# Kernel tuning notes

Hardware: AMD Instinct MI355X
Metric: run time of the kernel (lower is better)

Reference implementation:

```python
import jax, jax.numpy as jnp
import numpy as np

B, N_PER, F = 8, 4096, 64
RATIO, RADIUS, K = 0.25, 0.2, 64
S = int(N_PER * RATIO)  # 1024 samples per cloud
NEG = -1e30


def setup_inputs() -> dict:
    key = jax.random.key(0)
    ks = jax.random.split(key, 8)
    pos = jax.random.uniform(ks[0], (B * N_PER, 3), dtype=jnp.float32)
    x = jax.random.normal(ks[1], (B * N_PER, F), dtype=jnp.float32)
    batch = jnp.repeat(jnp.arange(B, dtype=jnp.int32), N_PER)
    W1 = jax.random.normal(ks[2], (F + 3, 128), dtype=jnp.float32) * 0.05
    b1 = jnp.zeros((128,), jnp.float32)
    W2 = jax.random.normal(ks[3], (128, 128), dtype=jnp.float32) * 0.05
    b2 = jnp.zeros((128,), jnp.float32)
    W3 = jax.random.normal(ks[4], (128, 256), dtype=jnp.float32) * 0.05
    b3 = jnp.zeros((256,), jnp.float32)
    return {"x": x, "pos": pos, "batch": batch,
            "W1": W1, "b1": b1, "W2": W2, "b2": b2, "W3": W3, "b3": b3}


def _fps_single(p):
    """Farthest point sampling on one cloud p:[N,3] -> S int32 indices (seed idx 0)."""
    d0 = jnp.sum((p - p[0]) ** 2, axis=-1)  # [N]

    def step(min_d, _):
        nxt = jnp.argmax(min_d).astype(jnp.int32)
        d = jnp.sum((p - p[nxt]) ** 2, axis=-1)
        return jnp.minimum(min_d, d), nxt

    _, rest = jax.lax.scan(step, d0, None, length=S - 1)
    return jnp.concatenate([jnp.zeros((1,), jnp.int32), rest])


def reference(x, pos, batch, W1, b1, W2, b2, W3, b3):
    pos_b = pos.reshape(B, N_PER, 3)
    x_b = x.reshape(B, N_PER, F)
    batch_b = batch.reshape(B, N_PER)

    # --- FPS sampling (sequential scan, vmapped over clouds) ---
    idx = jax.vmap(_fps_single)(pos_b)                                  # [B,S]
    pos_s = jnp.take_along_axis(pos_b, idx[..., None], axis=1)          # [B,S,3]

    # --- radius neighbor search: nearest K within RADIUS (deterministic) ---
    d2 = jnp.sum((pos_s[:, :, None, :] - pos_b[:, None, :, :]) ** 2, -1)  # [B,S,N]
    neg = jnp.where(d2 <= RADIUS ** 2, -d2, NEG)
    vals, nbr = jax.lax.top_k(neg, K)                                   # [B,S,K]
    valid = vals > NEG / 2                                              # [B,S,K]

    # --- gather neighbor features / positions ---
    x_j = jnp.take_along_axis(x_b[:, None], nbr[..., None], axis=2)     # [B,S,K,F]
    pos_j = jnp.take_along_axis(pos_b[:, None], nbr[..., None], axis=2) # [B,S,K,3]
    rel = pos_j - pos_s[:, :, None, :]                                  # [B,S,K,3]

    # --- edge MLP (Lin+ReLU per PyG PointNetConv local_nn) ---
    h = jnp.concatenate([x_j, rel], axis=-1)                            # [B,S,K,F+3]
    h = jax.nn.relu(h @ W1 + b1)
    h = jax.nn.relu(h @ W2 + b2)
    h = jax.nn.relu(h @ W3 + b3)                                        # [B,S,K,256]

    # --- scatter-max aggregation over neighbors ---
    h = jnp.where(valid[..., None], h, NEG)
    out = jnp.max(h, axis=2)                                            # [B,S,256]
    out = jnp.where(out > NEG / 2, out, 0.0)

    x1 = out.reshape(B * S, -1)
    pos1 = pos_s.reshape(B * S, 3)
    batch1 = jnp.take_along_axis(batch_b, idx, axis=1).reshape(-1)
    return x1, pos1, batch1
```

## Files before the change

kernel.cpp:

```cpp
#include <hip/hip_runtime.h>
#include <hip/hip_bf16.h>
#include <stdint.h>

#define NPER 4096
#define NCLOUD 8
#define FD 64
#define SS 1024
#define NBK 64
#define CAP 512

typedef unsigned int u32;
typedef unsigned long long u64;
typedef __attribute__((ext_vector_type(8))) short short8v;
typedef __attribute__((ext_vector_type(8))) unsigned short ushort8v;
typedef __attribute__((ext_vector_type(4))) float f32x4;

__device__ __forceinline__ float fadd(float a, float b){ return __fadd_rn(a,b); }
__device__ __forceinline__ float fsub(float a, float b){ return __fsub_rn(a,b); }
__device__ __forceinline__ float fmul(float a, float b){ return __fmul_rn(a,b); }
__device__ __forceinline__ float dist2(float ax,float ay,float az,float bx,float by,float bz){
  float dx=fsub(ax,bx), dy=fsub(ay,by), dz=fsub(az,bz);
  return fadd(fadd(fmul(dx,dx),fmul(dy,dy)),fmul(dz,dz));
}
__device__ __forceinline__ unsigned short f2b(float v){
  __hip_bfloat16 h = __float2bfloat16(v);
  return *reinterpret_cast<unsigned short*>(&h);
}

template<int CTRL, int RMASK>
__device__ __forceinline__ float dppmaxf(float v){
  int t = __builtin_amdgcn_update_dpp(0, __float_as_int(v), CTRL, RMASK, 0xf, false);
  return fmaxf(v, __int_as_float(t));
}

#define LOADG(q, j0, j1, j2, j3) { \
    const float4* pv = (const float4*)(pb + (size_t)(base + q*4)*3); \
    float4 v0=pv[0], v1=pv[1], v2=pv[2]; \
    x##j0=v0.x; y##j0=v0.y; z##j0=v0.z; \
    x##j1=v0.w; y##j1=v1.x; z##j1=v1.y; \
    x##j2=v1.z; y##j2=v1.w; z##j2=v2.x; \
    x##j3=v2.y; y##j3=v2.z; z##j3=v2.w; \
    float4 c0; c0.x=x##j0; c0.y=y##j0; c0.z=z##j0; c0.w=0.f; spt[base+q*4+0]=c0; \
    float4 c1; c1.x=x##j1; c1.y=y##j1; c1.z=z##j1; c1.w=0.f; spt[base+q*4+1]=c1; \
    float4 c2; c2.x=x##j2; c2.y=y##j2; c2.z=z##j2; c2.w=0.f; spt[base+q*4+2]=c2; \
    float4 c3; c3.x=x##j3; c3.y=y##j3; c3.z=z##j3; c3.w=0.f; spt[base+q*4+3]=c3; \
  }
#define DINIT(j) m##j = dist2(x##j,y##j,z##j,p0x,p0y,p0z);
#define DUPD(j)  { float d = dist2(x##j,y##j,z##j,pnx,pny,pnz); m##j = fminf(m##j,d); }
#define ARGMAX16() { \
      bool c; float w0,w1,w2,w3,w4,w5,w6,w7; int i0,i1,i2,i3,i4,i5,i6,i7; \
      c=m1>m0;   w0=c?m1:m0;   i0=base+(c?1:0); \
      c=m3>m2;   w1=c?m3:m2;   i1=base+(c?3:2); \
      c=m5>m4;   w2=c?m5:m4;   i2=base+(c?5:4); \
      c=m7>m6;   w3=c?m7:m6;   i3=base+(c?7:6); \
      c=m9>m8;   w4=c?m9:m8;   i4=base+(c?9:8); \
      c=m11>m10; w5=c?m11:m10; i5=base+(c?11:10); \
      c=m13>m12; w6=c?m13:m12; i6=base+(c?13:12); \
      c=m15>m14; w7=c?m15:m14; i7=base+(c?15:14); \
      c=w1>w0; w0=c?w1:w0; i0=c?i1:i0; \
      c=w3>w2; w2=c?w3:w2; i2=c?i3:i2; \
      c=w5>w4; w4=c?w5:w4; i4=c?i5:i4; \
      c=w7>w6; w6=c?w7:w6; i6=c?i7:i6; \
      c=w2>w0; w0=c?w2:w0; i0=c?i2:i0; \
      c=w6>w4; w4=c?w6:w4; i4=c?i6:i4; \
      c=w4>w0; bv=c?w4:w0; bidx=c?i4:i0; \
    }
#define FPS_ITER(IT, WX, WY, WZ) { \
    float rv = bv; \
    rv = dppmaxf<0x121,0xf>(rv); \
    rv = dppmaxf<0x122,0xf>(rv); \
    rv = dppmaxf<0x124,0xf>(rv); \
    rv = dppmaxf<0x128,0xf>(rv); \
    rv = dppmaxf<0x142,0xa>(rv); \
    rv = dppmaxf<0x143,0xc>(rv); \
    const float wv = __int_as_float(__builtin_amdgcn_readlane(__float_as_int(rv), 63)); \
    u64 em = __ballot(bv == wv); \
    const int wl = __ffsll(em) - 1; \
    const int par = (IT) & 1; \
    const u32 se = (u32)((IT) >> 1); \
    if (lane == wl) \
      skey[par][w] = ((u64)__float_as_uint(wv)<<32) | ((u64)se<<12) | (u64)(u32)(4095 - bidx); \
    u64 k0,k1,k2,k3; \
    for (;;) { \
      k0 = skey[par][0]; k1 = skey[par][1]; k2 = skey[par][2]; k3 = skey[par][3]; \
      u32 c0 = (((u32)k0)>>12)^se, c1 = (((u32)k1)>>12)^se; \
      u32 c2 = (((u32)k2)>>12)^se, c3 = (((u32)k3)>>12)^se; \
      if ((c0|c1|c2|c3) == 0u) break; \
    } \
    u64 ka = k0>k1?k0:k1, kb2 = k2>k3?k2:k3; \
    u64 km = ka>kb2?ka:kb2; \
    const int nxt = 4095 - (int)(km & 0xFFFull); \
    const float4 c = spt[nxt]; \
    const float pnx = __int_as_float(__builtin_amdgcn_readfirstlane(__float_as_int(c.x))); \
    const float pny = __int_as_float(__builtin_amdgcn_readfirstlane(__float_as_int(c.y))); \
    const float pnz = __int_as_float(__builtin_amdgcn_readfirstlane(__float_as_int(c.z))); \
    const bool mine = (t == ((IT) & 255)); \
    WX = mine ? pnx : WX; \
    WY = mine ? pny : WY; \
    WZ = mine ? pnz : WZ; \
    DUPD(0) DUPD(1) DUPD(2) DUPD(3) DUPD(4) DUPD(5) DUPD(6) DUPD(7) \
    DUPD(8) DUPD(9) DUPD(10) DUPD(11) DUPD(12) DUPD(13) DUPD(14) DUPD(15) \
    ARGMAX16() \
  }

__global__ __launch_bounds__(256, 1) void k_fps(const float* __restrict__ pos,
    float* __restrict__ pos_s, float* __restrict__ out_pos1, float* __restrict__ out_b1){
  __shared__ __align__(16) float4 spt[NPER];
  __shared__ volatile __align__(16) u64 skey[2][4];
  const int b = blockIdx.x;
  const int t = threadIdx.x;
  const int w = t >> 6, lane = t & 63;
  const float* pb = pos + (size_t)b*NPER*3;
  const int base = t*16;
  float x0,x1,x2,x3,x4,x5,x6,x7,x8,x9,x10,x11,x12,x13,x14,x15;
  float y0,y1,y2,y3,y4,y5,y6,y7,y8,y9,y10,y11,y12,y13,y14,y15;
  float z0,z1,z2,z3,z4,z5,z6,z7,z8,z9,z10,z11,z12,z13,z14,z15;
  float m0,m1,m2,m3,m4,m5,m6,m7,m8,m9,m10,m11,m12,m13,m14,m15;
  LOADG(0, 0, 1, 2, 3)
  LOADG(1, 4, 5, 6, 7)
  LOADG(2, 8, 9, 10, 11)
  LOADG(3, 12, 13, 14, 15)
  const float p0x=pb[0], p0y=pb[1], p0z=pb[2];
  DINIT(0) DINIT(1) DINIT(2) DINIT(3) DINIT(4) DINIT(5) DINIT(6) DINIT(7)
  DINIT(8) DINIT(9) DINIT(10) DINIT(11) DINIT(12) DINIT(13) DINIT(14) DINIT(15)
  float bv; int bidx;
  ARGMAX16()
  if (t < 8) skey[t>>2][t&3] = 0xFFFFF000ull;
  float wx0=p0x, wy0=p0y, wz0=p0z;
  float wx1=0.f, wy1=0.f, wz1=0.f;
  float wx2=0.f, wy2=0.f, wz2=0.f;
  float wx3=0.f, wy3=0.f, wz3=0.f;
  for (int i=t;i<SS;i+=256) out_b1[b*SS+i] = (float)b;
  __syncthreads();
  for (int it=1;   it<256;  ++it) FPS_ITER(it, wx0, wy0, wz0)
  for (int it=256; it<512;  ++it) FPS_ITER(it, wx1, wy1, wz1)
  for (int it=512; it<768;  ++it) FPS_ITER(it, wx2, wy2, wz2)
  for (int it=768; it<1024; ++it) FPS_ITER(it, wx3, wy3, wz3)
  {
    const size_t g = (size_t)b*SS;
    size_t o = (g + t)*3;
    pos_s[o]=wx0; pos_s[o+1]=wy0; pos_s[o+2]=wz0;
    out_pos1[o]=wx0; out_pos1[o+1]=wy0; out_pos1[o+2]=wz0;
    o = (g + 256 + t)*3;
    pos_s[o]=wx1; pos_s[o+1]=wy1; pos_s[o+2]=wz1;
    out_pos1[o]=wx1; out_pos1[o+1]=wy1; out_pos1[o+2]=wz1;
    o = (g + 512 + t)*3;
    pos_s[o]=wx2; pos_s[o+1]=wy2; pos_s[o+2]=wz2;
    out_pos1[o]=wx2; out_pos1[o+1]=wy2; out_pos1[o+2]=wz2;
    o = (g + 768 + t)*3;
    pos_s[o]=wx3; pos_s[o+1]=wy3; pos_s[o+2]=wz3;
    out_pos1[o]=wx3; out_pos1[o+1]=wy3; out_pos1[o+2]=wz3;
  }
}

__global__ __launch_bounds__(256) void k_nbr(const float* __restrict__ pos,
    const float* __restrict__ pos_s, unsigned short* __restrict__ nbr){
  __shared__ float sxx[NPER], syy[NPER], szz[NPER];
  __shared__ u64 lst[4][CAP];
  __shared__ int cnt[4];
  const int t = threadIdx.x;
  const int w = t>>6, lane = t&63;
  const int gid0 = blockIdx.x*4;
  const int b = gid0 >> 10;
  const float* pb = pos + (size_t)b*NPER*3;
  for (int i=t;i<NPER;i+=256){
    sxx[i]=pb[i*3+0]; syy[i]=pb[i*3+1]; szz[i]=pb[i*3+2];
  }
  if (t<4) cnt[t]=0;
  __syncthreads();
  const int gid = gid0 + w;
  const float qx=pos_s[(size_t)gid*3+0], qy=pos_s[(size_t)gid*3+1], qz=pos_s[(size_t)gid*3+2];
  for (int i0=0;i0<NPER;i0+=64){
    int p = i0 + lane;
    float d = dist2(qx,qy,qz,sxx[p],syy[p],szz[p]);
    bool in = (d <= 0.04f);
    u64 m = __ballot(in);
    if (m){
      int tot = __popcll(m);
      int bse = 0;
      if (lane==0) bse = atomicAdd(&cnt[w], tot);
      bse = __shfl(bse, 0, 64);
      if (in){
        int o = bse + __popcll(m & ((1ull<<lane)-1ull));
        if (o < CAP) lst[w][o] = ((u64)__float_as_uint(d)<<12) | (u64)(u32)p;
      }
    }
  }
  int n = cnt[w];
  if (n > CAP) n = CAP;
  unsigned short outv = 0xFFFFu;
  if (n <= 64){
    if (lane < n) outv = (unsigned short)(lst[w][lane] & 0xFFFull);
  } else {
    for (int r=0;r<64;++r){
      u64 bk = ~0ull; int bp = -1;
      for (int i=lane;i<n;i+=64){
        u64 v = lst[w][i];
        bool lt = v < bk;
        bk = lt ? v : bk;
        bp = lt ? i : bp;
      }
      u64 rk = bk;
      #pragma unroll
      for (int off=32; off>=1; off>>=1){
        u64 o = __shfl_xor(rk, off, 64);
        rk = (o < rk) ? o : rk;
      }
      if (bk == rk) lst[w][bp] = ~0ull;
      if (lane == r) outv = (unsigned short)(rk & 0xFFFull);
    }
  }
  nbr[(size_t)gid*NBK + lane] = outv;
}

__global__ __launch_bounds__(256) void k_wconv(const float* __restrict__ W1,
    const float* __restrict__ W2, const float* __restrict__ W3,
    unsigned short* __restrict__ Wt1, unsigned short* __restrict__ Wt2,
    unsigned short* __restrict__ Wt3){
  int t = blockIdx.x*256 + threadIdx.x;
  if (t < 16384){
    int n = t>>7, k = t&127;
    Wt1[t] = f2b(k < 67 ? W1[k*128+n] : 0.f);
  } else if (t < 32768){
    int q = t - 16384; int n = q>>7, k = q&127;
    Wt2[q] = f2b(W2[k*128+n]);
  } else if (t < 65536){
    int q = t - 32768; int n = q>>7, k = q&127;
    Wt3[q] = f2b(W3[k*256+n]);
  }
}

__device__ __forceinline__ void load_w(const unsigned short* __restrict__ src,
    unsigned short* __restrict__ wb, int t){
  const int n = t>>1, hf = t&1;
  const char* srow = (const char*)(src + n*128 + hf*64);
  char* drow = (char*)wb + n*256;
  const u32 sw = (u32)(n&7)<<4;
  #pragma unroll
  for (int c=0;c<8;c++){
    ushort8v v = *(const ushort8v*)(srow + c*16);
    u32 colbyte = (u32)hf*128 + (u32)c*16;
    *(ushort8v*)(drow + (colbyte ^ sw)) = v;
  }
}

__device__ __forceinline__ void zero_acc(f32x4 acc[4][4]){
  #pragma unroll
  for (int i=0;i<4;i++){
    #pragma unroll
    for (int j=0;j<4;j++){
      f32x4 z = {0.f,0.f,0.f,0.f};
      acc[i][j] = z;
    }
  }
}

__device__ __forceinline__ void gemm_wave(const unsigned short* __restrict__ wb,
    const unsigned short* __restrict__ hb, int nh, int lane, int ksteps, f32x4 acc[4][4]){
  const int li = lane & 15;
  const int lg = lane >> 4;
  for (int kk=0; kk<ksteps; ++kk){
    const u32 colb = (u32)(kk*64 + lg*16);
    short8v af[4], bfv[4];
    #pragma unroll
    for (int mt=0;mt<4;mt++){
      int wr = nh*64 + mt*16 + li;
      af[mt] = *(const short8v*)((const char*)wb + wr*256 + (colb ^ ((u32)(wr&7)<<4)));
    }
    #pragma unroll
    for (int nt=0;nt<4;nt++){
      int er = nt*16 + li;
      bfv[nt] = *(const short8v*)((const char*)hb + er*256 + (colb ^ ((u32)(er&7)<<4)));
    }
    #pragma unroll
    for (int mt=0;mt<4;mt++){
      #pragma unroll
      for (int nt=0;nt<4;nt++){
        acc[mt][nt] = __builtin_amdgcn_mfma_f32_16x16x32_bf16(af[mt], bfv[nt], acc[mt][nt], 0, 0, 0);
      }
    }
  }
}

__device__ __forceinline__ void epi_store(f32x4 acc[4][4], const float* __restrict__ bias,
    unsigned short* __restrict__ hb, int nh, int lane){
  const int li = lane & 15;
  const int lg = lane >> 4;
  #pragma unroll
  for (int mt=0;mt<4;mt++){
    const int c0 = nh*64 + mt*16 + lg*4;
    const float4 bb = *(const float4*)(bias + c0);
    #pragma unroll
    for (int nt=0;nt<4;nt++){
      const int r = nt*16 + li;
      f32x4 a = acc[mt][nt];
      float v0 = fmaxf(a.x + bb.x, 0.f);
      float v1 = fmaxf(a.y + bb.y, 0.f);
      float v2 = fmaxf(a.z + bb.z, 0.f);
      float v3 = fmaxf(a.w + bb.w, 0.f);
      u64 pk = (u64)f2b(v0) | ((u64)f2b(v1)<<16) | ((u64)f2b(v2)<<32) | ((u64)f2b(v3)<<48);
      u32 colbyte = (u32)(c0*2);
      *(u64*)((char*)hb + r*256 + (colbyte ^ ((u32)(r&7)<<4))) = pk;
    }
  }
}

__device__ __forceinline__ void epi_out(f32x4 acc[4][4], const float* __restrict__ b3g,
    float* __restrict__ outx, u64 vmask, int pass, int nh, int lane, int gs){
  const int li = lane & 15;
  const int lg = lane >> 4;
  #pragma unroll
  for (int mt=0;mt<4;mt++){
    const int c0 = pass*128 + nh*64 + mt*16 + lg*4;
    const float4 bb = *(const float4*)(b3g + c0);
    float vals[4];
    #pragma unroll
    for (int i=0;i<4;i++){
      float v = -1e30f;
      #pragma unroll
      for (int nt=0;nt<4;nt++){
        const int r = nt*16 + li;
        const bool ok = (vmask >> r) & 1ull;
        const float a = acc[mt][nt][i];
        v = fmaxf(v, ok ? a : -1e30f);
      }
      #pragma unroll
      for (int off=1; off<16; off<<=1){
        v = fmaxf(v, __shfl_xor(v, off, 64));
      }
      float biasv = (i==0)?bb.x:((i==1)?bb.y:((i==2)?bb.z:bb.w));
      vals[i] = fmaxf(v + biasv, 0.f);
    }
    if (li==0){
      float4 o; o.x=vals[0]; o.y=vals[1]; o.z=vals[2]; o.w=vals[3];
      *(float4*)(outx + (size_t)gs*256 + c0) = o;
    }
  }
}

__global__ __launch_bounds__(256) void k_mlp(const float* __restrict__ xg,
    const float* __restrict__ pg, const float* __restrict__ pos_s,
    const unsigned short* __restrict__ nbrg,
    const unsigned short* __restrict__ Wt1, const unsigned short* __restrict__ Wt2,
    const unsigned short* __restrict__ Wt3,
    const float* __restrict__ b1g, const float* __restrict__ b2g,
    const float* __restrict__ b3g, float* __restrict__ outx){
  __shared__ __align__(16) unsigned short hbuf[2][64][128];
  __shared__ __align__(16) unsigned short wbuf[128*128];
  __shared__ float spos[2][4];
  __shared__ unsigned short snbr[2][64];
  __shared__ u64 svalid[2];
  const int t = threadIdx.x;
  const int s0 = blockIdx.x*2;
  const int b = s0 >> 10;
  {
    u64* p = (u64*)hbuf;
    #pragma unroll
    for (int i=0;i<16;i++) p[t + i*256] = 0ull;
  }
  if (t < 2){
    spos[t][0]=pos_s[(size_t)(s0+t)*3+0];
    spos[t][1]=pos_s[(size_t)(s0+t)*3+1];
    spos[t][2]=pos_s[(size_t)(s0+t)*3+2];
  }
  if (t < 128){
    const int s=t>>6, r=t&63;
    unsigned short nb = nbrg[(size_t)(s0+s)*NBK + r];
    snbr[s][r]=nb;
    u64 m = __ballot(nb != 0xFFFFu);
    if (r==0) svalid[s]=m;
  }
  __syncthreads();
  {
    const int s = t>>7, r=(t>>1)&63, hf=t&1;
    const unsigned short nb = snbr[s][r];
    char* drow = (char*)hbuf + (s*64+r)*256;
    const u32 sw = (u32)(r&7)<<4;
    if (nb != 0xFFFFu){
      const float4* xr = (const float4*)(xg + ((size_t)b*NPER + nb)*FD + hf*32);
      #pragma unroll
      for (int c=0;c<4;c++){
        float4 v0 = xr[2*c];
        float4 v1 = xr[2*c+1];
        ushort8v u;
        u[0]=f2b(v0.x); u[1]=f2b(v0.y); u[2]=f2b(v0.z); u[3]=f2b(v0.w);
        u[4]=f2b(v1.x); u[5]=f2b(v1.y); u[6]=f2b(v1.z); u[7]=f2b(v1.w);
        u32 colbyte = (u32)hf*64 + (u32)c*16;
        *(ushort8v*)(drow + (colbyte ^ sw)) = u;
      }
      if (hf){
        const size_t po = ((size_t)b*NPER + nb)*3;
        float rx = fsub(pg[po+0], spos[s][0]);
        float ry = fsub(pg[po+1], spos[s][1]);
        float rz = fsub(pg[po+2], spos[s][2]);
        u64 pk = (u64)f2b(rx) | ((u64)f2b(ry)<<16) | ((u64)f2b(rz)<<32);
        *(u64*)(drow + (128u ^ sw)) = pk;
      }
    }
  }
  load_w(Wt1, wbuf, t);
  __syncthreads();
  const int w = t>>6, lane = t&63;
  const int s = w>>1, nh = w&1;
  unsigned short* hb = &hbuf[s][0][0];
  f32x4 acc[4][4];
  zero_acc(acc);
  gemm_wave(wbuf, hb, nh, lane, 3, acc);
  __syncthreads();
  epi_store(acc, b1g, hb, nh, lane);
  load_w(Wt2, wbuf, t);
  __syncthreads();
  zero_acc(acc);
  gemm_wave(wbuf, hb, nh, lane, 4, acc);
  __syncthreads();
  epi_store(acc, b2g, hb, nh, lane);
  load_w(Wt3, wbuf, t);
  __syncthreads();
  zero_acc(acc);
  gemm_wave(wbuf, hb, nh, lane, 4, acc);
  const u64 vm = svalid[s];
  epi_out(acc, b3g, outx, vm, 0, nh, lane, s0+s);
  __syncthreads();
  load_w(Wt3 + 128*128, wbuf, t);
  __syncthreads();
  zero_acc(acc);
  gemm_wave(wbuf, hb, nh, lane, 4, acc);
  epi_out(acc, b3g, outx, vm, 1, nh, lane, s0+s);
}

extern "C" void kernel_launch(void* const* d_in, const int* in_sizes, int n_in,
                              void* d_out, int out_size, void* d_ws, size_t ws_size,
                              hipStream_t stream) {
  (void)in_sizes; (void)n_in; (void)out_size; (void)ws_size;
  const float* xg = (const float*)d_in[0];
  const float* pg = (const float*)d_in[1];
  const float* W1 = (const float*)d_in[3];
  const float* b1 = (const float*)d_in[4];
  const float* W2 = (const float*)d_in[5];
  const float* b2 = (const float*)d_in[6];
  const float* W3 = (const float*)d_in[7];
  const float* b3 = (const float*)d_in[8];
  float* outx = (float*)d_out;
  float* outp = outx + (size_t)8192*256;
  float* outb = outp + (size_t)8192*3;
  char* ws = (char*)d_ws;
  float* pos_s = (float*)ws;
  unsigned short* nbr = (unsigned short*)(ws + 98304);
  unsigned short* Wt1 = (unsigned short*)(ws + 98304 + 1048576);
  unsigned short* Wt2 = Wt1 + 16384;
  unsigned short* Wt3 = Wt2 + 16384;
  hipLaunchKernelGGL(k_fps, dim3(NCLOUD), dim3(256), 0, stream, pg, pos_s, outp, outb);
  hipLaunchKernelGGL(k_wconv, dim3(256), dim3(256), 0, stream, W1, W2, W3, Wt1, Wt2, Wt3);
  hipLaunchKernelGGL(k_nbr, dim3(8192/4), dim3(256), 0, stream, pg, pos_s, nbr);
  hipLaunchKernelGGL(k_mlp, dim3(8192/2), dim3(256), 0, stream,
                     xg, pg, pos_s, nbr, Wt1, Wt2, Wt3, b1, b2, b3, outx);
}
```

Measured before the change: 1.086 ms.

## Use barrier-based FPS reduction, fuse weight conversion, register top-k for neighbors

Replaces the volatile spin-wait on sequence-tagged shared keys in the FPS loop with a __syncthreads barrier per iteration. The weight bf16 conversion kernel is merged into the FPS launch as extra blocks to remove a launch. The neighbor selection gains a register-resident path for up to 256 candidates using a DPP-based 64-bit wave min, avoiding repeated LDS scans. The barrier per FPS step may cost more or less than spinning.

```diff
diff --git a/kernel.cpp b/kernel.cpp
--- a/kernel.cpp
+++ b/kernel.cpp
@@ -31,6 +31,14 @@
 __device__ __forceinline__ float dppmaxf(float v){
   int t = __builtin_amdgcn_update_dpp(0, __float_as_int(v), CTRL, RMASK, 0xf, false);
   return fmaxf(v, __int_as_float(t));
+}
+template<int CTRL, int RMASK>
+__device__ __forceinline__ void kmin_stage(u32& hi, u32& lo){
+  u32 hio = (u32)__builtin_amdgcn_update_dpp(-1, (int)hi, CTRL, RMASK, 0xf, false);
+  u32 loo = (u32)__builtin_amdgcn_update_dpp(-1, (int)lo, CTRL, RMASK, 0xf, false);
+  u64 ko = ((u64)hio<<32)|loo, k = ((u64)hi<<32)|lo;
+  bool g = ko < k;
+  hi = g?hio:hi; lo = g?loo:lo;
 }
 
 #define LOADG(q, j0, j1, j2, j3) { \
@@ -77,16 +85,11 @@
     u64 em = __ballot(bv == wv); \
     const int wl = __ffsll(em) - 1; \
     const int par = (IT) & 1; \
-    const u32 se = (u32)((IT) >> 1); \
     if (lane == wl) \
-      skey[par][w] = ((u64)__float_as_uint(wv)<<32) | ((u64)se<<12) | (u64)(u32)(4095 - bidx); \
-    u64 k0,k1,k2,k3; \
-    for (;;) { \
-      k0 = skey[par][0]; k1 = skey[par][1]; k2 = skey[par][2]; k3 = skey[par][3]; \
-      u32 c0 = (((u32)k0)>>12)^se, c1 = (((u32)k1)>>12)^se; \
-      u32 c2 = (((u32)k2)>>12)^se, c3 = (((u32)k3)>>12)^se; \
-      if ((c0|c1|c2|c3) == 0u) break; \
-    } \
+      skey[par][w] = ((u64)__float_as_uint(wv)<<32) | (u64)(u32)(4095 - bidx); \
+    __syncthreads(); \
+    const u64* kp = &skey[par][0]; \
+    u64 k0=kp[0], k1=kp[1], k2=kp[2], k3=kp[3]; \
     u64 ka = k0>k1?k0:k1, kb2 = k2>k3?k2:k3; \
     u64 km = ka>kb2?ka:kb2; \
     const int nxt = 4095 - (int)(km & 0xFFFull); \
@@ -104,9 +107,26 @@
   }
 
 __global__ __launch_bounds__(256, 1) void k_fps(const float* __restrict__ pos,
-    float* __restrict__ pos_s, float* __restrict__ out_pos1, float* __restrict__ out_b1){
+    float* __restrict__ pos_s, float* __restrict__ out_pos1, float* __restrict__ out_b1,
+    const float* __restrict__ W1, const float* __restrict__ W2, const float* __restrict__ W3,
+    unsigned short* __restrict__ Wt1, unsigned short* __restrict__ Wt2,
+    unsigned short* __restrict__ Wt3){
   __shared__ __align__(16) float4 spt[NPER];
-  __shared__ volatile __align__(16) u64 skey[2][4];
+  __shared__ __align__(16) u64 skey[2][4];
+  if (blockIdx.x >= NCLOUD){
+    int tt = (int)(blockIdx.x - NCLOUD)*256 + (int)threadIdx.x;
+    if (tt < 16384){
+      int n = tt>>7, k = tt&127;
+      Wt1[tt] = f2b(k < 67 ? W1[k*128+n] : 0.f);
+    } else if (tt < 32768){
+      int q = tt - 16384; int n = q>>7, k = q&127;
+      Wt2[q] = f2b(W2[k*128+n]);
+    } else if (tt < 65536){
+      int q = tt - 32768; int n = q>>7, k = q&127;
+      Wt3[q] = f2b(W3[k*256+n]);
+    }
+    return;
+  }
   const int b = blockIdx.x;
   const int t = threadIdx.x;
   const int w = t >> 6, lane = t & 63;
@@ -125,7 +145,6 @@
   DINIT(8) DINIT(9) DINIT(10) DINIT(11) DINIT(12) DINIT(13) DINIT(14) DINIT(15)
   float bv; int bidx;
   ARGMAX16()
-  if (t < 8) skey[t>>2][t&3] = 0xFFFFF000ull;
   float wx0=p0x, wy0=p0y, wz0=p0z;
   float wx1=0.f, wy1=0.f, wz1=0.f;
   float wx2=0.f, wy2=0.f, wz2=0.f;
@@ -153,6 +172,19 @@
   }
 }
 
+__device__ __forceinline__ u64 wave_min_u64(u64 k){
+  u32 hi = (u32)(k>>32), lo = (u32)k;
+  kmin_stage<0x121,0xf>(hi,lo);
+  kmin_stage<0x122,0xf>(hi,lo);
+  kmin_stage<0x124,0xf>(hi,lo);
+  kmin_stage<0x128,0xf>(hi,lo);
+  kmin_stage<0x142,0xa>(hi,lo);
+  kmin_stage<0x143,0xc>(hi,lo);
+  u32 rhi = (u32)__builtin_amdgcn_readlane((int)hi, 63);
+  u32 rlo = (u32)__builtin_amdgcn_readlane((int)lo, 63);
+  return ((u64)rhi<<32) | rlo;
+}
+
 __global__ __launch_bounds__(256) void k_nbr(const float* __restrict__ pos,
     const float* __restrict__ pos_s, unsigned short* __restrict__ nbr){
   __shared__ float sxx[NPER], syy[NPER], szz[NPER];
@@ -191,6 +223,23 @@
   unsigned short outv = 0xFFFFu;
   if (n <= 64){
     if (lane < n) outv = (unsigned short)(lst[w][lane] & 0xFFFull);
+  } else if (n <= 256){
+    u64 c0=~0ull, c1=~0ull, c2=~0ull, c3=~0ull;
+    c0 = lst[w][lane];
+    if (lane+64  < n) c1 = lst[w][lane+64];
+    if (lane+128 < n) c2 = lst[w][lane+128];
+    if (lane+192 < n) c3 = lst[w][lane+192];
+    for (int r=0;r<64;++r){
+      u64 a  = c0<c1?c0:c1; int ia = c0<c1?0:1;
+      u64 b2 = c2<c3?c2:c3; int ib = c2<c3?2:3;
+      u64 bk = a<b2?a:b2;   int bp = a<b2?ia:ib;
+      u64 rk = wave_min_u64(bk);
+      if (bk == rk){
+        if (bp==0) c0=~0ull; else if (bp==1) c1=~0ull;
+        else if (bp==2) c2=~0ull; else c3=~0ull;
+      }
+      if (lane == r) outv = (unsigned short)(rk & 0xFFFull);
+    }
   } else {
     for (int r=0;r<64;++r){
       u64 bk = ~0ull; int bp = -1;
@@ -211,23 +260,6 @@
     }
   }
   nbr[(size_t)gid*NBK + lane] = outv;
-}
-
-__global__ __launch_bounds__(256) void k_wconv(const float* __restrict__ W1,
-    const float* __restrict__ W2, const float* __restrict__ W3,
-    unsigned short* __restrict__ Wt1, unsigned short* __restrict__ Wt2,
-    unsigned short* __restrict__ Wt3){
-  int t = blockIdx.x*256 + threadIdx.x;
-  if (t < 16384){
-    int n = t>>7, k = t&127;
-    Wt1[t] = f2b(k < 67 ? W1[k*128+n] : 0.f);
-  } else if (t < 32768){
-    int q = t - 16384; int n = q>>7, k = q&127;
-    Wt2[q] = f2b(W2[k*128+n]);
-  } else if (t < 65536){
-    int q = t - 32768; int n = q>>7, k = q&127;
-    Wt3[q] = f2b(W3[k*256+n]);
-  }
 }
 
 __device__ __forceinline__ void load_w(const unsigned short* __restrict__ src,
@@ -449,8 +481,8 @@
   unsigned short* Wt1 = (unsigned short*)(ws + 98304 + 1048576);
   unsigned short* Wt2 = Wt1 + 16384;
   unsigned short* Wt3 = Wt2 + 16384;
-  hipLaunchKernelGGL(k_fps, dim3(NCLOUD), dim3(256), 0, stream, pg, pos_s, outp, outb);
-  hipLaunchKernelGGL(k_wconv, dim3(256), dim3(256), 0, stream, W1, W2, W3, Wt1, Wt2, Wt3);
+  hipLaunchKernelGGL(k_fps, dim3(NCLOUD + 256), dim3(256), 0, stream,
+                     pg, pos_s, outp, outb, W1, W2, W3, Wt1, Wt2, Wt3);
   hipLaunchKernelGGL(k_nbr, dim3(8192/4), dim3(256), 0, stream, pg, pos_s, nbr);
   hipLaunchKernelGGL(k_mlp, dim3(8192/2), dim3(256), 0, stream,
                      xg, pg, pos_s, nbr, Wt1, Wt2, Wt3, b1, b2, b3, outx);
```

Measured after the change: 914.8 us. 15.8% less time.
